# Performance work log

Hardware: AMD Instinct MI355X
Metric: run time of the kernel (lower is better)

Reference implementation:

```python
import jax, jax.numpy as jnp
import numpy as np

N_NODES = 50000
N_EDGES = 800000
N_GRAPHS = 512
IN_DIM = 128
HID = 64
NLAYERS = 3
BN_EPS = 1e-5
NEG_SLOPE = 0.2


def setup_inputs() -> dict:
    key = jax.random.key(0)
    ks = jax.random.split(key, 16)
    s = 0.1  # weight scale
    x = jax.random.normal(ks[0], (N_NODES, IN_DIM), jnp.float32)
    ei_sc = jax.random.randint(ks[1], (2, N_EDGES), 0, N_NODES, dtype=jnp.int32)
    ei_fc = jax.random.randint(ks[2], (2, N_EDGES), 0, N_NODES, dtype=jnp.int32)
    batch_ids = jnp.sort(jax.random.randint(ks[3], (N_NODES,), 0, N_GRAPHS, dtype=jnp.int32))
    return {
        "x": x,
        "ei_sc": ei_sc,
        "ei_fc": ei_fc,
        "batch_ids": batch_ids,
        "Ws": jax.random.normal(ks[4], (NLAYERS, IN_DIM, 2 * HID), jnp.float32) * s,
        "att_src": jax.random.normal(ks[5], (NLAYERS, 2, HID), jnp.float32) * s,
        "att_dst": jax.random.normal(ks[6], (NLAYERS, 2, HID), jnp.float32) * s,
        "bgat": jnp.zeros((NLAYERS, 2 * HID), jnp.float32),
        "bn_g": jnp.ones((NLAYERS, 2 * HID), jnp.float32),
        "bn_b": jnp.zeros((NLAYERS, 2 * HID), jnp.float32),
        "Wf": jax.random.normal(ks[7], (2 * HID, HID), jnp.float32) * s,
        "af_src": jax.random.normal(ks[8], (1, HID), jnp.float32) * s,
        "af_dst": jax.random.normal(ks[9], (1, HID), jnp.float32) * s,
        "bf": jnp.zeros((HID,), jnp.float32),
        "Wo": jax.random.normal(ks[10], (HID, 1), jnp.float32) * s,
        "bo": jnp.zeros((1,), jnp.float32),
    }


def gat_conv(x, src, dst, W, a_src, a_dst, b):
    """PyG GATConv: linear -> per-head attention logits -> dst-segment softmax -> scatter-sum."""
    N = x.shape[0]
    H, C = a_src.shape
    h = (x @ W).reshape(N, H, C)                      # [N,H,C]
    loop = jnp.arange(N, dtype=src.dtype)             # add self-loops (PyG default)
    s = jnp.concatenate([src, loop])
    d = jnp.concatenate([dst, loop])
    al_s = jnp.einsum('nhc,hc->nh', h, a_src)         # [N,H]
    al_d = jnp.einsum('nhc,hc->nh', h, a_dst)
    al = jax.nn.leaky_relu(al_s[s] + al_d[d], NEG_SLOPE)  # [E,H]
    m = jax.ops.segment_max(al, d, num_segments=N)
    m = jnp.where(jnp.isfinite(m), m, 0.0)
    e = jnp.exp(al - m[d])
    denom = jax.ops.segment_sum(e, d, num_segments=N)
    coef = e / (denom[d] + 1e-16)                     # softmax over incoming edges
    out = jax.ops.segment_sum(coef[:, :, None] * h[s], d, num_segments=N)  # [N,H,C]
    return out.reshape(N, H * C) + b                  # concat heads + bias


def batch_norm(x, g, b):
    mu = x.mean(axis=0)
    var = ((x - mu) ** 2).mean(axis=0)                # biased var, as torch BN train-mode
    return (x - mu) * jax.lax.rsqrt(var + BN_EPS) * g + b


def reference(x, ei_sc, ei_fc, batch_ids, Ws, att_src, att_dst, bgat,
              bn_g, bn_b, Wf, af_src, af_dst, bf, Wo, bo):
    x0 = x
    x1 = x
    for l in range(NLAYERS):
        x0 = gat_conv(x0, ei_sc[0], ei_sc[1], Ws[l], att_src[l], att_dst[l], bgat[l])
        x1 = gat_conv(x1, ei_fc[0], ei_fc[1], Ws[l], att_src[l], att_dst[l], bgat[l])
        x0 = jax.nn.relu(batch_norm(x0, bn_g[l], bn_b[l]))
        x1 = jax.nn.relu(batch_norm(x1, bn_g[l], bn_b[l]))
        # Dropout: identity (eval mode, deterministic reference)
    x0 = gat_conv(x0, ei_sc[0], ei_sc[1], Wf, af_src, af_dst, bf)
    x1 = gat_conv(x1, ei_fc[0], ei_fc[1], Wf, af_src, af_dst, bf)
    xf = (x0 + x1) * 0.5                              # reduce_fuse_embed='mean'
    out = xf @ Wo + bo                                # [N, nclass]
    sums = jax.ops.segment_sum(out, batch_ids, num_segments=N_GRAPHS)
    cnts = jax.ops.segment_sum(jnp.ones((out.shape[0], 1), out.dtype), batch_ids, num_segments=N_GRAPHS)
    return sums / jnp.maximum(cnts, 1.0)              # scatter mean over graphs -> [G, nclass]
```

## Files before the change

kernel.cpp:

```cpp
#include <hip/hip_runtime.h>
#include <cstdint>
#include <cstddef>


#define NLAYERS 3

__device__ __forceinline__ float lrelu(float a){ return a > 0.f ? a : 0.2f*a; }

__device__ __forceinline__ float wsum(float v){
#pragma unroll
  for (int o = 32; o > 0; o >>= 1) v += __shfl_xor(v, o);
  return v;
}
__device__ __forceinline__ int rdl_i(int v, int l){ return __builtin_amdgcn_readlane(v, l); }
__device__ __forceinline__ float rdl_f(float v, int l){
  return __uint_as_float(__builtin_amdgcn_readlane(__float_as_uint(v), l));
}

__global__ void zero_k(int* __restrict__ p, int n){
  int i = blockIdx.x*blockDim.x + threadIdx.x;
  if (i < n) p[i] = 0;
}
__global__ void copy_k(const int* __restrict__ a, int* __restrict__ b, int n){
  int i = blockIdx.x*blockDim.x + threadIdx.x;
  if (i < n) b[i] = a[i];
}
__global__ void count_k(const int* __restrict__ dst, int E, int* __restrict__ cnt){
  int e = blockIdx.x*blockDim.x + threadIdx.x;
  if (e < E) atomicAdd(&cnt[dst[e]], 1);
}
__global__ __launch_bounds__(1024) void scanA_k(const int* __restrict__ cnt,
    int* __restrict__ excl, int* __restrict__ bsum, int N){
  __shared__ int wpart[16];
  const int tid = threadIdx.x, lane = tid & 63, w = tid >> 6;
  const int i = blockIdx.x*1024 + tid;
  const int v = (i < N) ? cnt[i] : 0;
  int s = v;
#pragma unroll
  for (int o = 1; o < 64; o <<= 1){ int t = __shfl_up(s, o); if (lane >= o) s += t; }
  if (lane == 63) wpart[w] = s;
  __syncthreads();
  if (w == 0){
    int t = (lane < 16) ? wpart[lane] : 0;
#pragma unroll
    for (int o = 1; o < 16; o <<= 1){ int u = __shfl_up(t, o); if (lane >= o) t += u; }
    if (lane < 16) wpart[lane] = t;
  }
  __syncthreads();
  const int woff = (w > 0) ? wpart[w-1] : 0;
  const int incl = s + woff;
  if (i < N) excl[i] = incl - v;
  if (tid == 1023) bsum[blockIdx.x] = incl;
}
__global__ void scanB_k(const int* __restrict__ bsum, int* __restrict__ boff, int nb){
  const int lane = threadIdx.x;
  const int v = (lane < nb) ? bsum[lane] : 0;
  int s = v;
#pragma unroll
  for (int o = 1; o < 64; o <<= 1){ int t = __shfl_up(s, o); if (lane >= o) s += t; }
  if (lane < nb) boff[lane] = s - v;
  if (lane == nb-1) boff[nb] = s;
}
__global__ __launch_bounds__(1024) void scanC_k(int* __restrict__ rp,
    const int* __restrict__ boff, int N, int nb){
  const int i = blockIdx.x*1024 + threadIdx.x;
  if (i < N) rp[i] += boff[blockIdx.x];
  if (i == 0) rp[N] = boff[nb];
}
__global__ void fill_k(const int* __restrict__ src, const int* __restrict__ dst, int E,
                       int* __restrict__ pos, int* __restrict__ col){
  int e = blockIdx.x*blockDim.x + threadIdx.x;
  if (e < E){
    int d = dst[e];
    int p = atomicAdd(&pos[d], 1);
    col[p] = src[e];
  }
}

__global__ __launch_bounds__(256) void gemm_k(const float* __restrict__ A,
    const float* __restrict__ W, float* __restrict__ O,
    const float* __restrict__ bnsc, const float* __restrict__ bnsh,
    const float* __restrict__ atts, const float* __restrict__ attd,
    float* __restrict__ als, float* __restrict__ ald, int N, int M){
  __shared__ float xs[128][64];
  __shared__ float wsh[128][64];
  const int tid = threadIdx.x;
  const int row0 = blockIdx.x*64, col0 = blockIdx.y*64;
  const int HS = gridDim.y;
  {
    const int c4 = (tid & 15)*4;
#pragma unroll
    for (int p = 0; p < 8; ++p){
      const int k = p*16 + (tid >> 4);
      *reinterpret_cast<float4*>(&wsh[k][c4]) =
          *reinterpret_cast<const float4*>(&W[(size_t)k*M + col0 + c4]);
    }
    const int k4 = (tid & 31)*4;
    const int rbase = (tid >> 5);
#pragma unroll
    for (int p = 0; p < 8; ++p){
      const int rr = p*8 + rbase;
      int gr = row0 + rr; if (gr > N-1) gr = N-1;
      float4 xv = *reinterpret_cast<const float4*>(&A[(size_t)gr*128 + k4]);
      float xq[4] = {xv.x, xv.y, xv.z, xv.w};
      if (bnsc != nullptr){
#pragma unroll
        for (int q = 0; q < 4; ++q)
          xq[q] = fmaxf(xq[q]*bnsc[k4 + q] + bnsh[k4 + q], 0.f);
      }
#pragma unroll
      for (int q = 0; q < 4; ++q){
        const int k = k4 + q;
        const int swz = ((k >> 2) & 15) << 2;
        xs[k][rr ^ swz] = xq[q];
      }
    }
  }
  __syncthreads();
  const int ty = tid >> 4, tx = tid & 15;
  float acc[4][4] = {};
#pragma unroll 8
  for (int k = 0; k < 128; ++k){
    const int swz = ((k >> 2) & 15) << 2;
    const int xr = (ty*4) ^ swz;
    const float4 xv = *reinterpret_cast<const float4*>(&xs[k][xr]);
    const float2 w0 = *reinterpret_cast<const float2*>(&wsh[k][2*tx]);
    const float2 w1 = *reinterpret_cast<const float2*>(&wsh[k][32 + 2*tx]);
    const float xq[4] = {xv.x, xv.y, xv.z, xv.w};
#pragma unroll
    for (int i = 0; i < 4; ++i){
      acc[i][0] += xq[i]*w0.x;
      acc[i][1] += xq[i]*w0.y;
      acc[i][2] += xq[i]*w1.x;
      acc[i][3] += xq[i]*w1.y;
    }
  }
  {
    const float* as = atts + col0;
    const float* ad = attd + col0;
    const float a_s0 = as[2*tx],      a_s1 = as[2*tx + 1];
    const float a_s2 = as[32 + 2*tx], a_s3 = as[33 + 2*tx];
    const float a_d0 = ad[2*tx],      a_d1 = ad[2*tx + 1];
    const float a_d2 = ad[32 + 2*tx], a_d3 = ad[33 + 2*tx];
#pragma unroll
    for (int i = 0; i < 4; ++i){
      float ps = acc[i][0]*a_s0 + acc[i][1]*a_s1 + acc[i][2]*a_s2 + acc[i][3]*a_s3;
      float pd = acc[i][0]*a_d0 + acc[i][1]*a_d1 + acc[i][2]*a_d2 + acc[i][3]*a_d3;
#pragma unroll
      for (int o = 1; o < 16; o <<= 1){
        ps += __shfl_xor(ps, o);
        pd += __shfl_xor(pd, o);
      }
      const int r = row0 + ty*4 + i;
      if (tx == 0 && r < N){
        als[(size_t)r*HS + blockIdx.y] = ps;
        ald[(size_t)r*HS + blockIdx.y] = pd;
      }
    }
  }
#pragma unroll
  for (int i = 0; i < 4; ++i){
    const int r = row0 + ty*4 + i;
    if (r < N){
      float2* o2 = reinterpret_cast<float2*>(&O[(size_t)r*M + col0]);
      o2[tx]      = make_float2(acc[i][0], acc[i][1]);
      o2[16 + tx] = make_float2(acc[i][2], acc[i][3]);
    }
  }
}

template<int H>
__global__ __launch_bounds__(256) void agg_k(const float* __restrict__ h,
    const float* __restrict__ als, const float* __restrict__ ald,
    const int* __restrict__ rp, const int* __restrict__ col,
    const float* __restrict__ bias, float* __restrict__ out, int N){
  const int lane = threadIdx.x & 63;
  const int n = blockIdx.x*4 + (threadIdx.x >> 6);
  if (n >= N) return;
  const int beg = rp[n], end = rp[n+1];
  float as0, as1 = 0.f, ad0, ad1 = 0.f;
  if (H == 2){
    const float2 a = ((const float2*)als)[n];
    const float2 d = ((const float2*)ald)[n];
    as0 = a.x; as1 = a.y; ad0 = d.x; ad1 = d.y;
  } else { as0 = als[n]; ad0 = ald[n]; }
  const float self0 = lrelu(as0 + ad0);
  const float self1 = (H == 2) ? lrelu(as1 + ad1) : 0.f;
  float m0 = self0, p0 = (lane == 0) ? 1.f : 0.f;
  float m1 = self1, p1 = (lane == 0) ? 1.f : 0.f;
  for (int i = beg + lane; i < end; i += 64){
    const int s = col[i];
    if (H == 2){
      const float2 a = ((const float2*)als)[s];
      const float al0 = lrelu(a.x + ad0);
      const float al1 = lrelu(a.y + ad1);
      if (al0 > m0){ p0 = p0*__expf(m0 - al0) + 1.f; m0 = al0; }
      else p0 += __expf(al0 - m0);
      if (al1 > m1){ p1 = p1*__expf(m1 - al1) + 1.f; m1 = al1; }
      else p1 += __expf(al1 - m1);
    } else {
      const float al0 = lrelu(als[s] + ad0);
      if (al0 > m0){ p0 = p0*__expf(m0 - al0) + 1.f; m0 = al0; }
      else p0 += __expf(al0 - m0);
    }
  }
#pragma unroll
  for (int o = 1; o < 64; o <<= 1){
    const float om0 = __shfl_xor(m0, o), op0 = __shfl_xor(p0, o);
    const float nm0 = fmaxf(m0, om0);
    p0 = p0*__expf(m0 - nm0) + op0*__expf(om0 - nm0); m0 = nm0;
    if (H == 2){
      const float om1 = __shfl_xor(m1, o), op1 = __shfl_xor(p1, o);
      const float nm1 = fmaxf(m1, om1);
      p1 = p1*__expf(m1 - nm1) + op1*__expf(om1 - nm1); m1 = nm1;
    }
  }
  const float inv0 = 1.f/(p0 + 1e-16f);
  const float inv1 = (H == 2) ? 1.f/(p1 + 1e-16f) : 0.f;

  if (H == 2){
    const float2* h2 = (const float2*)h;
    const float csel = (lane < 32) ? __expf(self0 - m0)*inv0 : __expf(self1 - m1)*inv1;
    const float2 hv = h2[(size_t)n*64 + lane];
    float ax = csel*hv.x, ay = csel*hv.y;
    for (int base = beg; base < end; base += 64){
      const int idx = base + lane;
      int sv = 0; float c0v = 0.f, c1v = 0.f;
      if (idx < end){
        sv = col[idx];
        const float2 a = ((const float2*)als)[sv];
        c0v = __expf(lrelu(a.x + ad0) - m0)*inv0;
        c1v = __expf(lrelu(a.y + ad1) - m1)*inv1;
      }
      const int cnt = min(64, end - base);
      for (int j = 0; j < cnt; ++j){
        const int s = rdl_i(sv, j);
        const float c0 = rdl_f(c0v, j);
        const float c1 = rdl_f(c1v, j);
        const float c = (lane < 32) ? c0 : c1;
        const float2 hvv = h2[(size_t)s*64 + lane];
        ax += c*hvv.x; ay += c*hvv.y;
      }
    }
    const float2 bv = ((const float2*)bias)[lane];
    ((float2*)out)[(size_t)n*64 + lane] = make_float2(ax + bv.x, ay + bv.y);
  } else {
    const float csel = __expf(self0 - m0)*inv0;
    float a0 = csel*h[(size_t)n*64 + lane];
    for (int base = beg; base < end; base += 64){
      const int idx = base + lane;
      int sv = 0; float c0v = 0.f;
      if (idx < end){
        sv = col[idx];
        c0v = __expf(lrelu(als[sv] + ad0) - m0)*inv0;
      }
      const int cnt = min(64, end - base);
      for (int j = 0; j < cnt; ++j){
        const int s = rdl_i(sv, j);
        const float c = rdl_f(c0v, j);
        a0 += c*h[(size_t)s*64 + lane];
      }
    }
    out[(size_t)n*64 + lane] = a0 + bias[lane];
  }
}

__global__ __launch_bounds__(128) void bn_stats_k(const float* __restrict__ x, int N,
                                                  double* __restrict__ st){
  const int c = threadIdx.x;
  double s = 0.0, s2 = 0.0;
  for (int r = blockIdx.x; r < N; r += gridDim.x){
    const float v = x[(size_t)r*128 + c];
    s += v; s2 += (double)v*(double)v;
  }
  atomicAdd(&st[c], s);
  atomicAdd(&st[128 + c], s2);
}
__global__ __launch_bounds__(128) void bnfin_k(const double* __restrict__ st,
    const float* __restrict__ g, const float* __restrict__ b,
    float* __restrict__ sc, float* __restrict__ sh, int N){
  const int c = threadIdx.x;
  const double mu  = st[c]/(double)N;
  const double var = st[128 + c]/(double)N - mu*mu;
  const float s = rsqrtf((float)var + 1e-5f)*g[c];
  sc[c] = s;
  sh[c] = b[c] - (float)mu*s;
}

__global__ __launch_bounds__(256) void pred_k(const float* __restrict__ f0,
    const float* __restrict__ f1, const float* __restrict__ Wo,
    float* __restrict__ pred, int N){
  const int lane = threadIdx.x & 63;
  const int n = blockIdx.x*4 + (threadIdx.x >> 6);
  if (n >= N) return;
  const float xf = (f0[(size_t)n*64 + lane] + f1[(size_t)n*64 + lane])*0.5f;
  const float p = wsum(xf*Wo[lane]);
  if (lane == 0) pred[n] = p;
}
__global__ __launch_bounds__(64) void segred_k(const float* __restrict__ pred,
    const int* __restrict__ bid, const float* __restrict__ bo,
    float* __restrict__ out, int N){
  const int g = blockIdx.x;
  int lo = 0, hi = N;
  while (lo < hi){ const int mid = (lo + hi) >> 1; if (bid[mid] < g) lo = mid + 1; else hi = mid; }
  const int s0 = lo;
  hi = N;
  while (lo < hi){ const int mid = (lo + hi) >> 1; if (bid[mid] < g + 1) lo = mid + 1; else hi = mid; }
  const int s1 = lo;
  float s = 0.f;
  for (int i = s0 + threadIdx.x; i < s1; i += 64) s += pred[i];
  s = wsum(s);
  if (threadIdx.x == 0)
    out[g] = (s1 > s0) ? s/(float)(s1 - s0) + bo[0] : 0.f;
}

extern "C" void kernel_launch(void* const* d_in, const int* in_sizes, int n_in,
                              void* d_out, int out_size, void* d_ws, size_t ws_size,
                              hipStream_t stream) {
  const int N = in_sizes[0]/128;
  const int E = in_sizes[1]/2;
  const int G = out_size;

  const float* x    = (const float*)d_in[0];
  const int*   eisc = (const int*)d_in[1];
  const int*   eifc = (const int*)d_in[2];
  const int*   bid  = (const int*)d_in[3];
  const float* Ws   = (const float*)d_in[4];
  const float* atts = (const float*)d_in[5];
  const float* attd = (const float*)d_in[6];
  const float* bgat = (const float*)d_in[7];
  const float* bng  = (const float*)d_in[8];
  const float* bnb  = (const float*)d_in[9];
  const float* Wf   = (const float*)d_in[10];
  const float* afs  = (const float*)d_in[11];
  const float* afd  = (const float*)d_in[12];
  const float* bf   = (const float*)d_in[13];
  const float* Wo   = (const float*)d_in[14];
  const float* bo   = (const float*)d_in[15];
  float* out = (float*)d_out;

  char* wp = (char*)d_ws;
  auto grab = [&](size_t bytes)->char* {
    uintptr_t p = ((uintptr_t)wp + 255) & ~(uintptr_t)255;
    wp = (char*)(p + bytes);
    return (char*)p;
  };
  char* zbase = (char*)(((uintptr_t)d_ws + 255) & ~(uintptr_t)255);
  int*    cntA  = (int*)grab((size_t)N*4);
  int*    cntB  = (int*)grab((size_t)N*4);
  double* stats = (double*)grab((size_t)6*256*8);
  const int zwords = (int)(((size_t)(wp - zbase)) / 4);
  int*   rp_sc  = (int*)grab((size_t)(N+1)*4);
  int*   rp_fc  = (int*)grab((size_t)(N+1)*4);
  int*   col_sc = (int*)grab((size_t)E*4);
  int*   col_fc = (int*)grab((size_t)E*4);
  int*   bsum   = (int*)grab(64*4);
  int*   boff   = (int*)grab(65*4);
  float* hb     = (float*)grab((size_t)N*128*4);
  float* x0b    = (float*)grab((size_t)N*128*4);
  float* x1b    = (float*)grab((size_t)N*128*4);
  float* alsb   = (float*)grab((size_t)N*2*4);
  float* aldb   = (float*)grab((size_t)N*2*4);
  float* bnsc   = (float*)grab((size_t)6*128*4);
  float* bnsh   = (float*)grab((size_t)6*128*4);
  float* pred   = alsb;
  (void)ws_size; (void)n_in;

  zero_k<<<(zwords + 255)/256, 256, 0, stream>>>((int*)zbase, zwords);

  const int EB = (E + 255)/256;
  const int SB = (N + 1023)/1024;
  count_k<<<EB, 256, 0, stream>>>(eisc + E, E, cntA);
  count_k<<<EB, 256, 0, stream>>>(eifc + E, E, cntB);
  scanA_k<<<SB, 1024, 0, stream>>>(cntA, rp_sc, bsum, N);
  scanB_k<<<1, 64, 0, stream>>>(bsum, boff, SB);
  scanC_k<<<SB, 1024, 0, stream>>>(rp_sc, boff, N, SB);
  copy_k<<<(N + 255)/256, 256, 0, stream>>>(rp_sc, cntA, N);
  fill_k<<<EB, 256, 0, stream>>>(eisc, eisc + E, E, cntA, col_sc);
  scanA_k<<<SB, 1024, 0, stream>>>(cntB, rp_fc, bsum, N);
  scanB_k<<<1, 64, 0, stream>>>(bsum, boff, SB);
  scanC_k<<<SB, 1024, 0, stream>>>(rp_fc, boff, N, SB);
  copy_k<<<(N + 255)/256, 256, 0, stream>>>(rp_fc, cntB, N);
  fill_k<<<EB, 256, 0, stream>>>(eifc, eifc + E, E, cntB, col_fc);

  const int NB4 = (N + 3)/4;
  const dim3 gg2((N + 63)/64, 2), gg1((N + 63)/64, 1);
  const float* cur0 = x;
  const float* cur1 = x;
  for (int l = 0; l < NLAYERS; ++l){
    const float* Wl = Ws + (size_t)l*128*128;
    const float* as = atts + l*128;
    const float* ad = attd + l*128;
    const float* bg = bgat + l*128;
    const float* sc0 = (l == 0) ? nullptr : bnsc + ((l-1)*2 + 0)*128;
    const float* sh0 = (l == 0) ? nullptr : bnsh + ((l-1)*2 + 0)*128;
    const float* sc1 = (l == 0) ? nullptr : bnsc + ((l-1)*2 + 1)*128;
    const float* sh1 = (l == 0) ? nullptr : bnsh + ((l-1)*2 + 1)*128;

    gemm_k<<<gg2, 256, 0, stream>>>(cur0, Wl, hb, sc0, sh0, as, ad, alsb, aldb, N, 128);
    agg_k<2><<<NB4, 256, 0, stream>>>(hb, alsb, aldb, rp_sc, col_sc, bg, x0b, N);
    bn_stats_k<<<512, 128, 0, stream>>>(x0b, N, stats + (l*2 + 0)*256);
    bnfin_k<<<1, 128, 0, stream>>>(stats + (l*2 + 0)*256, bng + l*128, bnb + l*128,
                                   bnsc + (l*2 + 0)*128, bnsh + (l*2 + 0)*128, N);
    if (l != 0)
      gemm_k<<<gg2, 256, 0, stream>>>(cur1, Wl, hb, sc1, sh1, as, ad, alsb, aldb, N, 128);
    agg_k<2><<<NB4, 256, 0, stream>>>(hb, alsb, aldb, rp_fc, col_fc, bg, x1b, N);
    bn_stats_k<<<512, 128, 0, stream>>>(x1b, N, stats + (l*2 + 1)*256);
    bnfin_k<<<1, 128, 0, stream>>>(stats + (l*2 + 1)*256, bng + l*128, bnb + l*128,
                                   bnsc + (l*2 + 1)*128, bnsh + (l*2 + 1)*128, N);
    cur0 = x0b;
    cur1 = x1b;
  }
  gemm_k<<<gg1, 256, 0, stream>>>(cur0, Wf, hb, bnsc + 4*128, bnsh + 4*128,
                                  afs, afd, alsb, aldb, N, 64);
  agg_k<1><<<NB4, 256, 0, stream>>>(hb, alsb, aldb, rp_sc, col_sc, bf, x0b, N);

  gemm_k<<<gg1, 256, 0, stream>>>(cur1, Wf, hb, bnsc + 5*128, bnsh + 5*128,
                                  afs, afd, alsb, aldb, N, 64);
  agg_k<1><<<NB4, 256, 0, stream>>>(hb, alsb, aldb, rp_fc, col_fc, bf, x1b, N);

  pred_k<<<NB4, 256, 0, stream>>>(x0b, x1b, Wo, pred, N);
  segred_k<<<G, 64, 0, stream>>>(pred, bid, bo, out, N);
}
```

Baseline: 1.346 ms.

## Sort CSR rows, widen aggregation gathers to float4, split GEMM K, deterministic BN reduction

Adds a per-row insertion sort of CSR column indices so neighbour gathers come out in order and results no longer depend on atomic fill order. The aggregation kernel now gathers float4 rows: several edges run in parallel across sub-groups of the wavefront, then a shuffle reduction combines them, cutting loop iterations per node. The GEMM tiles K in two halves to halve shared memory for higher occupancy. BatchNorm stats move from double atomics to per-block partials reduced by a multi-block finalize kernel. Fast __expf is swapped for expf, which may cost some throughput, and the sort adds a serial per-thread pass whose cost grows with node degree.

```diff
diff --git a/kernel.cpp b/kernel.cpp
--- a/kernel.cpp
+++ b/kernel.cpp
@@ -4,6 +4,7 @@
 
 
 #define NLAYERS 3
+#define BN_BLOCKS 256
 
 __device__ __forceinline__ float lrelu(float a){ return a > 0.f ? a : 0.2f*a; }
 
@@ -11,10 +12,6 @@
 #pragma unroll
   for (int o = 32; o > 0; o >>= 1) v += __shfl_xor(v, o);
   return v;
-}
-__device__ __forceinline__ int rdl_i(int v, int l){ return __builtin_amdgcn_readlane(v, l); }
-__device__ __forceinline__ float rdl_f(float v, int l){
-  return __uint_as_float(__builtin_amdgcn_readlane(__float_as_uint(v), l));
 }
 
 __global__ void zero_k(int* __restrict__ p, int n){
@@ -76,64 +73,81 @@
     col[p] = src[e];
   }
 }
+__global__ void sortrow_k(const int* __restrict__ rp, int* __restrict__ col, int N){
+  const int n = blockIdx.x*blockDim.x + threadIdx.x;
+  if (n >= N) return;
+  const int b = rp[n], e = rp[n+1];
+  for (int i = b + 1; i < e; ++i){
+    const int key = col[i];
+    int j = i - 1;
+    while (j >= b && col[j] > key){ col[j+1] = col[j]; --j; }
+    col[j+1] = key;
+  }
+}
 
 __global__ __launch_bounds__(256) void gemm_k(const float* __restrict__ A,
     const float* __restrict__ W, float* __restrict__ O,
     const float* __restrict__ bnsc, const float* __restrict__ bnsh,
     const float* __restrict__ atts, const float* __restrict__ attd,
     float* __restrict__ als, float* __restrict__ ald, int N, int M){
-  __shared__ float xs[128][64];
-  __shared__ float wsh[128][64];
+  __shared__ float xs[64][64];
+  __shared__ float wsh[64][64];
   const int tid = threadIdx.x;
   const int row0 = blockIdx.x*64, col0 = blockIdx.y*64;
   const int HS = gridDim.y;
-  {
-    const int c4 = (tid & 15)*4;
-#pragma unroll
-    for (int p = 0; p < 8; ++p){
-      const int k = p*16 + (tid >> 4);
-      *reinterpret_cast<float4*>(&wsh[k][c4]) =
-          *reinterpret_cast<const float4*>(&W[(size_t)k*M + col0 + c4]);
-    }
-    const int k4 = (tid & 31)*4;
-    const int rbase = (tid >> 5);
-#pragma unroll
-    for (int p = 0; p < 8; ++p){
-      const int rr = p*8 + rbase;
-      int gr = row0 + rr; if (gr > N-1) gr = N-1;
-      float4 xv = *reinterpret_cast<const float4*>(&A[(size_t)gr*128 + k4]);
-      float xq[4] = {xv.x, xv.y, xv.z, xv.w};
-      if (bnsc != nullptr){
-#pragma unroll
-        for (int q = 0; q < 4; ++q)
-          xq[q] = fmaxf(xq[q]*bnsc[k4 + q] + bnsh[k4 + q], 0.f);
-      }
-#pragma unroll
-      for (int q = 0; q < 4; ++q){
-        const int k = k4 + q;
-        const int swz = ((k >> 2) & 15) << 2;
-        xs[k][rr ^ swz] = xq[q];
-      }
-    }
-  }
-  __syncthreads();
   const int ty = tid >> 4, tx = tid & 15;
   float acc[4][4] = {};
+
+  for (int kk = 0; kk < 128; kk += 64){
+    {
+      const int c4 = (tid & 15)*4;
+#pragma unroll
+      for (int p = 0; p < 4; ++p){
+        const int k = p*16 + (tid >> 4);
+        *reinterpret_cast<float4*>(&wsh[k][c4]) =
+            *reinterpret_cast<const float4*>(&W[(size_t)(kk + k)*M + col0 + c4]);
+      }
+    }
+    {
+      const int k4 = (tid & 15)*4;
+      const int rbase = tid >> 4;
+#pragma unroll
+      for (int p = 0; p < 4; ++p){
+        const int rr = p*16 + rbase;
+        int gr = row0 + rr; if (gr > N-1) gr = N-1;
+        float4 xv = *reinterpret_cast<const float4*>(&A[(size_t)gr*128 + kk + k4]);
+        float xq[4] = {xv.x, xv.y, xv.z, xv.w};
+        if (bnsc != nullptr){
+#pragma unroll
+          for (int q = 0; q < 4; ++q)
+            xq[q] = fmaxf(xq[q]*bnsc[kk + k4 + q] + bnsh[kk + k4 + q], 0.f);
+        }
+#pragma unroll
+        for (int q = 0; q < 4; ++q){
+          const int k = k4 + q;
+          const int swz = ((k >> 2) & 15) << 2;
+          xs[k][rr ^ swz] = xq[q];
+        }
+      }
+    }
+    __syncthreads();
 #pragma unroll 8
-  for (int k = 0; k < 128; ++k){
-    const int swz = ((k >> 2) & 15) << 2;
-    const int xr = (ty*4) ^ swz;
-    const float4 xv = *reinterpret_cast<const float4*>(&xs[k][xr]);
-    const float2 w0 = *reinterpret_cast<const float2*>(&wsh[k][2*tx]);
-    const float2 w1 = *reinterpret_cast<const float2*>(&wsh[k][32 + 2*tx]);
-    const float xq[4] = {xv.x, xv.y, xv.z, xv.w};
-#pragma unroll
-    for (int i = 0; i < 4; ++i){
-      acc[i][0] += xq[i]*w0.x;
-      acc[i][1] += xq[i]*w0.y;
-      acc[i][2] += xq[i]*w1.x;
-      acc[i][3] += xq[i]*w1.y;
-    }
+    for (int k = 0; k < 64; ++k){
+      const int swz = ((k >> 2) & 15) << 2;
+      const int xr = (ty*4) ^ swz;
+      const float4 xv = *reinterpret_cast<const float4*>(&xs[k][xr]);
+      const float2 w0 = *reinterpret_cast<const float2*>(&wsh[k][2*tx]);
+      const float2 w1 = *reinterpret_cast<const float2*>(&wsh[k][32 + 2*tx]);
+      const float xq[4] = {xv.x, xv.y, xv.z, xv.w};
+#pragma unroll
+      for (int i = 0; i < 4; ++i){
+        acc[i][0] += xq[i]*w0.x;
+        acc[i][1] += xq[i]*w0.y;
+        acc[i][2] += xq[i]*w1.x;
+        acc[i][3] += xq[i]*w1.y;
+      }
+    }
+    __syncthreads();
   }
   {
     const float* as = atts + col0;
@@ -194,97 +208,134 @@
       const float2 a = ((const float2*)als)[s];
       const float al0 = lrelu(a.x + ad0);
       const float al1 = lrelu(a.y + ad1);
-      if (al0 > m0){ p0 = p0*__expf(m0 - al0) + 1.f; m0 = al0; }
-      else p0 += __expf(al0 - m0);
-      if (al1 > m1){ p1 = p1*__expf(m1 - al1) + 1.f; m1 = al1; }
-      else p1 += __expf(al1 - m1);
+      if (al0 > m0){ p0 = p0*expf(m0 - al0) + 1.f; m0 = al0; }
+      else p0 += expf(al0 - m0);
+      if (al1 > m1){ p1 = p1*expf(m1 - al1) + 1.f; m1 = al1; }
+      else p1 += expf(al1 - m1);
     } else {
       const float al0 = lrelu(als[s] + ad0);
-      if (al0 > m0){ p0 = p0*__expf(m0 - al0) + 1.f; m0 = al0; }
-      else p0 += __expf(al0 - m0);
+      if (al0 > m0){ p0 = p0*expf(m0 - al0) + 1.f; m0 = al0; }
+      else p0 += expf(al0 - m0);
     }
   }
 #pragma unroll
   for (int o = 1; o < 64; o <<= 1){
     const float om0 = __shfl_xor(m0, o), op0 = __shfl_xor(p0, o);
     const float nm0 = fmaxf(m0, om0);
-    p0 = p0*__expf(m0 - nm0) + op0*__expf(om0 - nm0); m0 = nm0;
+    p0 = p0*expf(m0 - nm0) + op0*expf(om0 - nm0); m0 = nm0;
     if (H == 2){
       const float om1 = __shfl_xor(m1, o), op1 = __shfl_xor(p1, o);
       const float nm1 = fmaxf(m1, om1);
-      p1 = p1*__expf(m1 - nm1) + op1*__expf(om1 - nm1); m1 = nm1;
+      p1 = p1*expf(m1 - nm1) + op1*expf(om1 - nm1); m1 = nm1;
     }
   }
   const float inv0 = 1.f/(p0 + 1e-16f);
   const float inv1 = (H == 2) ? 1.f/(p1 + 1e-16f) : 0.f;
 
+  const float4* h4 = (const float4*)h;
   if (H == 2){
-    const float2* h2 = (const float2*)h;
-    const float csel = (lane < 32) ? __expf(self0 - m0)*inv0 : __expf(self1 - m1)*inv1;
-    const float2 hv = h2[(size_t)n*64 + lane];
-    float ax = csel*hv.x, ay = csel*hv.y;
+    const int sub = lane & 31;
+    const int half = lane >> 5;
+    const float csel = (sub < 16) ? expf(self0 - m0)*inv0 : expf(self1 - m1)*inv1;
+    const float cs = (half == 0) ? csel : 0.f;
+    const float4 hv = h4[(size_t)n*32 + sub];
+    float ax = cs*hv.x, ay = cs*hv.y, az = cs*hv.z, aw = cs*hv.w;
     for (int base = beg; base < end; base += 64){
       const int idx = base + lane;
-      int sv = 0; float c0v = 0.f, c1v = 0.f;
+      int sv = n; float c0v = 0.f, c1v = 0.f;
       if (idx < end){
         sv = col[idx];
         const float2 a = ((const float2*)als)[sv];
-        c0v = __expf(lrelu(a.x + ad0) - m0)*inv0;
-        c1v = __expf(lrelu(a.y + ad1) - m1)*inv1;
+        c0v = expf(lrelu(a.x + ad0) - m0)*inv0;
+        c1v = expf(lrelu(a.y + ad1) - m1)*inv1;
       }
       const int cnt = min(64, end - base);
-      for (int j = 0; j < cnt; ++j){
-        const int s = rdl_i(sv, j);
-        const float c0 = rdl_f(c0v, j);
-        const float c1 = rdl_f(c1v, j);
-        const float c = (lane < 32) ? c0 : c1;
-        const float2 hvv = h2[(size_t)s*64 + lane];
-        ax += c*hvv.x; ay += c*hvv.y;
-      }
-    }
-    const float2 bv = ((const float2*)bias)[lane];
-    ((float2*)out)[(size_t)n*64 + lane] = make_float2(ax + bv.x, ay + bv.y);
+      const int iters = (cnt + 1) >> 1;
+      for (int j = 0; j < iters; ++j){
+        const int e = 2*j + half;
+        const int   src = __shfl(sv, e);
+        const float cc0 = __shfl(c0v, e);
+        const float cc1 = __shfl(c1v, e);
+        const float c = (sub < 16) ? cc0 : cc1;
+        const float4 hvv = h4[(size_t)src*32 + sub];
+        ax += c*hvv.x; ay += c*hvv.y; az += c*hvv.z; aw += c*hvv.w;
+      }
+    }
+    ax += __shfl_xor(ax, 32); ay += __shfl_xor(ay, 32);
+    az += __shfl_xor(az, 32); aw += __shfl_xor(aw, 32);
+    if (lane < 32){
+      const float4 bv = ((const float4*)bias)[sub];
+      float4 o4 = make_float4(ax + bv.x, ay + bv.y, az + bv.z, aw + bv.w);
+      ((float4*)out)[(size_t)n*32 + sub] = o4;
+    }
   } else {
-    const float csel = __expf(self0 - m0)*inv0;
-    float a0 = csel*h[(size_t)n*64 + lane];
+    const int sub = lane & 15;
+    const int quad = lane >> 4;
+    const float cs = (quad == 0) ? expf(self0 - m0)*inv0 : 0.f;
+    const float4 hv = h4[(size_t)n*16 + sub];
+    float ax = cs*hv.x, ay = cs*hv.y, az = cs*hv.z, aw = cs*hv.w;
     for (int base = beg; base < end; base += 64){
       const int idx = base + lane;
-      int sv = 0; float c0v = 0.f;
+      int sv = n; float c0v = 0.f;
       if (idx < end){
         sv = col[idx];
-        c0v = __expf(lrelu(als[sv] + ad0) - m0)*inv0;
+        c0v = expf(lrelu(als[sv] + ad0) - m0)*inv0;
       }
       const int cnt = min(64, end - base);
-      for (int j = 0; j < cnt; ++j){
-        const int s = rdl_i(sv, j);
-        const float c = rdl_f(c0v, j);
-        a0 += c*h[(size_t)s*64 + lane];
-      }
-    }
-    out[(size_t)n*64 + lane] = a0 + bias[lane];
+      const int iters = (cnt + 3) >> 2;
+      for (int j = 0; j < iters; ++j){
+        const int e = 4*j + quad;
+        const int   src = __shfl(sv, e);
+        const float cc  = __shfl(c0v, e);
+        const float4 hvv = h4[(size_t)src*16 + sub];
+        ax += cc*hvv.x; ay += cc*hvv.y; az += cc*hvv.z; aw += cc*hvv.w;
+      }
+    }
+    ax += __shfl_xor(ax, 16); ay += __shfl_xor(ay, 16);
+    az += __shfl_xor(az, 16); aw += __shfl_xor(aw, 16);
+    ax += __shfl_xor(ax, 32); ay += __shfl_xor(ay, 32);
+    az += __shfl_xor(az, 32); aw += __shfl_xor(aw, 32);
+    if (lane < 16){
+      const float4 bv = ((const float4*)bias)[sub];
+      float4 o4 = make_float4(ax + bv.x, ay + bv.y, az + bv.z, aw + bv.w);
+      ((float4*)out)[(size_t)n*16 + sub] = o4;
+    }
   }
 }
 
 __global__ __launch_bounds__(128) void bn_stats_k(const float* __restrict__ x, int N,
-                                                  double* __restrict__ st){
+                                                  double* __restrict__ part){
   const int c = threadIdx.x;
   double s = 0.0, s2 = 0.0;
   for (int r = blockIdx.x; r < N; r += gridDim.x){
     const float v = x[(size_t)r*128 + c];
     s += v; s2 += (double)v*(double)v;
   }
-  atomicAdd(&st[c], s);
-  atomicAdd(&st[128 + c], s2);
-}
-__global__ __launch_bounds__(128) void bnfin_k(const double* __restrict__ st,
+  part[(size_t)blockIdx.x*256 + c]       = s;
+  part[(size_t)blockIdx.x*256 + 128 + c] = s2;
+}
+__global__ __launch_bounds__(64) void bnfin_k(const double* __restrict__ part,
     const float* __restrict__ g, const float* __restrict__ b,
     float* __restrict__ sc, float* __restrict__ sh, int N){
-  const int c = threadIdx.x;
-  const double mu  = st[c]/(double)N;
-  const double var = st[128 + c]/(double)N - mu*mu;
-  const float s = rsqrtf((float)var + 1e-5f)*g[c];
-  sc[c] = s;
-  sh[c] = b[c] - (float)mu*s;
+  const int c = blockIdx.x;
+  const int l = threadIdx.x;
+  double s = 0.0, s2 = 0.0;
+  for (int i = l; i < BN_BLOCKS; i += 64){
+    s  += part[(size_t)i*256 + c];
+    s2 += part[(size_t)i*256 + 128 + c];
+  }
+#pragma unroll
+  for (int o = 32; o > 0; o >>= 1){
+    s  += __shfl_xor(s, o);
+    s2 += __shfl_xor(s2, o);
+  }
+  if (l == 0){
+    const double mu  = s/(double)N;
+    const double var = s2/(double)N - mu*mu;
+    const float scale = rsqrtf((float)var + 1e-5f)*g[c];
+    sc[c] = scale;
+    sh[c] = b[c] - (float)mu*scale;
+  }
 }
 
 __global__ __launch_bounds__(256) void pred_k(const float* __restrict__ f0,
@@ -348,8 +399,8 @@
   char* zbase = (char*)(((uintptr_t)d_ws + 255) & ~(uintptr_t)255);
   int*    cntA  = (int*)grab((size_t)N*4);
   int*    cntB  = (int*)grab((size_t)N*4);
-  double* stats = (double*)grab((size_t)6*256*8);
   const int zwords = (int)(((size_t)(wp - zbase)) / 4);
+  double* part  = (double*)grab((size_t)BN_BLOCKS*256*8);
   int*   rp_sc  = (int*)grab((size_t)(N+1)*4);
   int*   rp_fc  = (int*)grab((size_t)(N+1)*4);
   int*   col_sc = (int*)grab((size_t)E*4);
@@ -369,19 +420,22 @@
   zero_k<<<(zwords + 255)/256, 256, 0, stream>>>((int*)zbase, zwords);
 
   const int EB = (E + 255)/256;
+  const int NB = (N + 255)/256;
   const int SB = (N + 1023)/1024;
   count_k<<<EB, 256, 0, stream>>>(eisc + E, E, cntA);
   count_k<<<EB, 256, 0, stream>>>(eifc + E, E, cntB);
   scanA_k<<<SB, 1024, 0, stream>>>(cntA, rp_sc, bsum, N);
   scanB_k<<<1, 64, 0, stream>>>(bsum, boff, SB);
   scanC_k<<<SB, 1024, 0, stream>>>(rp_sc, boff, N, SB);
-  copy_k<<<(N + 255)/256, 256, 0, stream>>>(rp_sc, cntA, N);
+  copy_k<<<NB, 256, 0, stream>>>(rp_sc, cntA, N);
   fill_k<<<EB, 256, 0, stream>>>(eisc, eisc + E, E, cntA, col_sc);
+  sortrow_k<<<NB, 256, 0, stream>>>(rp_sc, col_sc, N);
   scanA_k<<<SB, 1024, 0, stream>>>(cntB, rp_fc, bsum, N);
   scanB_k<<<1, 64, 0, stream>>>(bsum, boff, SB);
   scanC_k<<<SB, 1024, 0, stream>>>(rp_fc, boff, N, SB);
-  copy_k<<<(N + 255)/256, 256, 0, stream>>>(rp_fc, cntB, N);
+  copy_k<<<NB, 256, 0, stream>>>(rp_fc, cntB, N);
   fill_k<<<EB, 256, 0, stream>>>(eifc, eifc + E, E, cntB, col_fc);
+  sortrow_k<<<NB, 256, 0, stream>>>(rp_fc, col_fc, N);
 
   const int NB4 = (N + 3)/4;
   const dim3 gg2((N + 63)/64, 2), gg1((N + 63)/64, 1);
@@ -399,15 +453,15 @@
 
     gemm_k<<<gg2, 256, 0, stream>>>(cur0, Wl, hb, sc0, sh0, as, ad, alsb, aldb, N, 128);
     agg_k<2><<<NB4, 256, 0, stream>>>(hb, alsb, aldb, rp_sc, col_sc, bg, x0b, N);
-    bn_stats_k<<<512, 128, 0, stream>>>(x0b, N, stats + (l*2 + 0)*256);
-    bnfin_k<<<1, 128, 0, stream>>>(stats + (l*2 + 0)*256, bng + l*128, bnb + l*128,
-                                   bnsc + (l*2 + 0)*128, bnsh + (l*2 + 0)*128, N);
+    bn_stats_k<<<BN_BLOCKS, 128, 0, stream>>>(x0b, N, part);
+    bnfin_k<<<128, 64, 0, stream>>>(part, bng + l*128, bnb + l*128,
+                                    bnsc + (l*2 + 0)*128, bnsh + (l*2 + 0)*128, N);
     if (l != 0)
       gemm_k<<<gg2, 256, 0, stream>>>(cur1, Wl, hb, sc1, sh1, as, ad, alsb, aldb, N, 128);
     agg_k<2><<<NB4, 256, 0, stream>>>(hb, alsb, aldb, rp_fc, col_fc, bg, x1b, N);
-    bn_stats_k<<<512, 128, 0, stream>>>(x1b, N, stats + (l*2 + 1)*256);
-    bnfin_k<<<1, 128, 0, stream>>>(stats + (l*2 + 1)*256, bng + l*128, bnb + l*128,
-                                   bnsc + (l*2 + 1)*128, bnsh + (l*2 + 1)*128, N);
+    bn_stats_k<<<BN_BLOCKS, 128, 0, stream>>>(x1b, N, part);
+    bnfin_k<<<128, 64, 0, stream>>>(part, bng + l*128, bnb + l*128,
+                                    bnsc + (l*2 + 1)*128, bnsh + (l*2 + 1)*128, N);
     cur0 = x0b;
     cur1 = x1b;
   }
```

After: 1.523 ms. +13.2%, slower.
